# Kernel tuning notes

Measured on AMD Instinct MI355X. Metric: run time of the kernel, lower is better.

## Reference

```python
import math
import jax, jax.numpy as jnp
import numpy as np

N, L, D = 64, 128, 768          # batch, n_in capsules, feature dim
IN_DIM, OUT_DIM, N_OUT = 64, 64, 32
EPS = 1e-8

def _xavier(k, shape):
    # torch xavier_uniform: fan_in = shape[1]*prod(shape[2:]), fan_out = shape[0]*prod(shape[2:])
    rec = int(np.prod(shape[2:])) if len(shape) > 2 else 1
    fan_in, fan_out = shape[-2] * rec, shape[-1] * rec
    a = math.sqrt(6.0 / (fan_in + fan_out))
    return jax.random.uniform(k, shape, jnp.float32, -a, a)

def setup_inputs() -> dict:
    key = jax.random.key(0)
    ks = jax.random.split(key, 4)
    return {
        "x": jax.random.normal(ks[0], (N, L, D), jnp.float32),
        "Wscore": _xavier(ks[1], (L, D, 1)),
        "Bscore": jnp.zeros((L, 1, 1), jnp.float32),
        "Wcap": _xavier(ks[2], (L, D, IN_DIM)),
        "Bcap": jnp.zeros((L, 1, IN_DIM), jnp.float32),
        "Wvote": _xavier(ks[3], (L, N_OUT, IN_DIM, OUT_DIM)),
        "Bvote": jnp.zeros((L, N_OUT, 1, OUT_DIM), jnp.float32),
        "beta_use": jnp.zeros((L, 1, 1, 1), jnp.float32),
        "beta_ign": jnp.zeros((1, N_OUT, 1, 1), jnp.float32),
        "iters": 3,
    }

def reference(x, Wscore, Bscore, Wcap, Bcap, Wvote, Bvote, beta_use, beta_ign, iters):
    n_out = Wvote.shape[1]
    pi = jnp.asarray(math.pi, x.dtype)
    x_t = jnp.transpose(x, (1, 0, 2))                     # (L, N, D)
    a_in = jnp.matmul(x_t, Wscore) + Bscore               # (L, N, 1)
    mu_in = jax.nn.gelu(jnp.matmul(x_t, Wcap) + Bcap, approximate=False)  # (L, N, in_dim)
    f_a_in = jax.nn.sigmoid(a_in)[:, None, :, :]          # (L, 1, N, 1)
    # votes: (L, n_out, N, out_dim)
    V = jnp.einsum('lni,loij->lonj', mu_in, Wvote) + Bvote

    def em_step(R):
        D_use = f_a_in * R                                # (L, n_out, N, 1)
        D_ign = f_a_in - D_use
        a_out = jnp.sum(beta_use * D_use, axis=0) - jnp.sum(beta_ign * D_ign, axis=0)  # (n_out, N, 1)
        denom = jnp.sum(D_use, axis=0) + EPS              # (n_out, N, 1)
        mu_out = jnp.sum(D_use * V, axis=0) / denom       # (n_out, N, out_dim)
        var_out = jnp.sum(D_use * (V - mu_out[None]) ** 2, axis=0) / denom
        return a_out, mu_out, var_out

    R = jnp.full((1, n_out, 1, 1), 1.0 / n_out, dtype=x.dtype)
    a_out, mu_out, var_out = em_step(R)
    for _ in range(int(iters) - 1):
        # Gaussian log-likelihood of each vote under each output capsule
        log_p = (-jnp.sum((V - mu_out[None]) ** 2 / (2.0 * var_out[None] + EPS), axis=-1)
                 - 1.0 - 0.5 * pi
                 - 0.5 * jnp.sum(jnp.log(var_out[None] + EPS), axis=-1))   # (L, n_out, N)
        R = jax.nn.softmax(jax.nn.log_sigmoid(a_out)[None] + log_p[..., None], axis=1)
        a_out, mu_out, var_out = em_step(R)

    a_out = jnp.transpose(a_out[..., 0], (1, 0))          # (N, n_out)
    mu_out = jnp.transpose(mu_out, (1, 0, 2))             # (N, n_out, out_dim)
    return a_out, mu_out
```

## Files before the change

kernel.cpp:

```cpp
#include <hip/hip_runtime.h>
#include <math.h>

#define NB 64
#define LL 128
#define DD 768
#define ID 64
#define OD 64
#define NO 32
#define EPSF 1e-8f


__device__ __forceinline__ float gelu_exact(float v) {
  return 0.5f * v * (1.0f + erff(v * 0.70710678118654752440f));
}
__device__ __forceinline__ float sigmoidf_(float z) {
  return 1.0f / (1.0f + __expf(-z));
}

__global__ __launch_bounds__(256) void k0a_proj(
    const float* __restrict__ x, const float* __restrict__ Wscore,
    const float* __restrict__ Wcap,
    float* __restrict__ Cpart, float* __restrict__ apart)
{
  const int l  = blockIdx.x & 127;
  const int kc = blockIdx.x >> 7;
  const int t = threadIdx.x;
  const int tn = t >> 4;
  const int ti = t & 15;
  __shared__ float Xs[64][68];
  __shared__ float Ws[64][68];
  __shared__ float Ss[64];
  float C[4][4] = {{0.f}};
  float asum[4] = {0.f, 0.f, 0.f, 0.f};

  for (int kt = 0; kt < 2; ++kt) {
    const int kbase = kc * 128 + kt * 64;
#pragma unroll
    for (int r = 0; r < 4; ++r) {
      const int flat = r * 1024 + t * 4;
      const int p = flat >> 6, qq = flat & 63;
      *(float4*)&Xs[p][qq] = *(const float4*)&x[(p * LL + l) * DD + kbase + qq];
      *(float4*)&Ws[p][qq] = *(const float4*)&Wcap[(l * DD + kbase + p) * ID + qq];
    }
    if (t < 16)
      *(float4*)&Ss[4 * t] = *(const float4*)&Wscore[l * DD + kbase + 4 * t];
    __syncthreads();
#pragma unroll 8
    for (int k = 0; k < 64; ++k) {
      float av[4];
      av[0] = Xs[4 * tn + 0][k];
      av[1] = Xs[4 * tn + 1][k];
      av[2] = Xs[4 * tn + 2][k];
      av[3] = Xs[4 * tn + 3][k];
      const float4 b = *(const float4*)&Ws[k][4 * ti];
      const float sk = Ss[k];
#pragma unroll
      for (int a = 0; a < 4; ++a) {
        C[a][0] = fmaf(av[a], b.x, C[a][0]);
        C[a][1] = fmaf(av[a], b.y, C[a][1]);
        C[a][2] = fmaf(av[a], b.z, C[a][2]);
        C[a][3] = fmaf(av[a], b.w, C[a][3]);
        asum[a] = fmaf(av[a], sk, asum[a]);
      }
    }
    __syncthreads();
  }
#pragma unroll
  for (int a = 0; a < 4; ++a)
    *(float4*)&Cpart[kc * 524288 + (l * 64 + 4 * tn + a) * 64 + 4 * ti] =
        make_float4(C[a][0], C[a][1], C[a][2], C[a][3]);
  if (ti == 0) {
#pragma unroll
    for (int a = 0; a < 4; ++a)
      apart[kc * 8192 + l * 64 + 4 * tn + a] = asum[a];
  }
}

__global__ __launch_bounds__(256) void k0b_reduce(
    const float* __restrict__ Cpart, const float* __restrict__ Bcap,
    float* __restrict__ mu_in)
{
  const int e = (blockIdx.x * 256 + threadIdx.x) * 4;
  float4 s = *(const float4*)&Cpart[e];
#pragma unroll
  for (int kc = 1; kc < 6; ++kc) {
    const float4 p = *(const float4*)&Cpart[kc * 524288 + e];
    s.x += p.x; s.y += p.y; s.z += p.z; s.w += p.w;
  }
  const int l = e >> 12;
  const int col = e & 63;
  const float4 bc = *(const float4*)&Bcap[l * 64 + col];
  float4 g;
  g.x = gelu_exact(s.x + bc.x);
  g.y = gelu_exact(s.y + bc.y);
  g.z = gelu_exact(s.z + bc.z);
  g.w = gelu_exact(s.w + bc.w);
  *(float4*)&mu_in[e] = g;
}

__global__ __launch_bounds__(256) void k0c_fa(
    const float* __restrict__ apart, const float* __restrict__ Bscore,
    float* __restrict__ f_a)
{
  const int e = blockIdx.x * 256 + threadIdx.x;
  float s = 0.f;
#pragma unroll
  for (int kc = 0; kc < 6; ++kc) s += apart[kc * 8192 + e];
  const int l = e >> 6;
  f_a[e] = sigmoidf_(s + Bscore[l]);
}

__global__ __launch_bounds__(256) void k1_votes(
    const float* __restrict__ mu_in, const float* __restrict__ Wvote,
    const float* __restrict__ Bvote, const float* __restrict__ f_a,
    float* __restrict__ V, float* __restrict__ S1p, float* __restrict__ S2p)
{
  const int o = blockIdx.x & 31;
  const int c = blockIdx.x >> 5;
  const int t = threadIdx.x;
  const int tn = t >> 4, tj = t & 15;
  __shared__ float As[64][68];
  __shared__ float Bs[64][68];
  float s1[4][4] = {{0.f}}, s2acc[4][4] = {{0.f}};

  for (int l = c * 8; l < c * 8 + 8; ++l) {
#pragma unroll
    for (int r = 0; r < 4; ++r) {
      const int flat = r * 1024 + t * 4;
      const int p = flat >> 6, qq = flat & 63;
      *(float4*)&As[p][qq] = *(const float4*)&mu_in[(l * NB + p) * ID + qq];
      *(float4*)&Bs[p][qq] = *(const float4*)&Wvote[((l * NO + o) * ID + p) * OD + qq];
    }
    __syncthreads();
    float C[4][4] = {{0.f}};
#pragma unroll 8
    for (int k = 0; k < 64; ++k) {
      float av[4];
      av[0] = As[4 * tn + 0][k];
      av[1] = As[4 * tn + 1][k];
      av[2] = As[4 * tn + 2][k];
      av[3] = As[4 * tn + 3][k];
      const float4 b = *(const float4*)&Bs[k][4 * tj];
#pragma unroll
      for (int a = 0; a < 4; ++a) {
        C[a][0] = fmaf(av[a], b.x, C[a][0]);
        C[a][1] = fmaf(av[a], b.y, C[a][1]);
        C[a][2] = fmaf(av[a], b.z, C[a][2]);
        C[a][3] = fmaf(av[a], b.w, C[a][3]);
      }
    }
    __syncthreads();
    const float4 bv = *(const float4*)&Bvote[(l * NO + o) * OD + 4 * tj];
    float wN[4];
#pragma unroll
    for (int a = 0; a < 4; ++a)
      wN[a] = f_a[l * NB + 4 * tn + a] * (1.0f / NO);
#pragma unroll
    for (int a = 0; a < 4; ++a) {
      float4 vv;
      vv.x = C[a][0] + bv.x;
      vv.y = C[a][1] + bv.y;
      vv.z = C[a][2] + bv.z;
      vv.w = C[a][3] + bv.w;
      *(float4*)&V[((4 * tn + a) * LL + l) * (NO * OD) + o * OD + 4 * tj] = vv;
      s1[a][0] = fmaf(wN[a], vv.x, s1[a][0]);
      s1[a][1] = fmaf(wN[a], vv.y, s1[a][1]);
      s1[a][2] = fmaf(wN[a], vv.z, s1[a][2]);
      s1[a][3] = fmaf(wN[a], vv.w, s1[a][3]);
      s2acc[a][0] = fmaf(wN[a] * vv.x, vv.x, s2acc[a][0]);
      s2acc[a][1] = fmaf(wN[a] * vv.y, vv.y, s2acc[a][1]);
      s2acc[a][2] = fmaf(wN[a] * vv.z, vv.z, s2acc[a][2]);
      s2acc[a][3] = fmaf(wN[a] * vv.w, vv.w, s2acc[a][3]);
    }
  }
#pragma unroll
  for (int a = 0; a < 4; ++a) {
    const int base = ((c * NB + 4 * tn + a) * NO + o) * OD + 4 * tj;
    *(float4*)&S1p[base] = make_float4(s1[a][0], s1[a][1], s1[a][2], s1[a][3]);
    *(float4*)&S2p[base] = make_float4(s2acc[a][0], s2acc[a][1], s2acc[a][2], s2acc[a][3]);
  }
}

__global__ __launch_bounds__(256) void k2_fin1(
    const float* __restrict__ S1p, const float* __restrict__ S2p,
    const float* __restrict__ f_a, const float* __restrict__ beta_use,
    const float* __restrict__ beta_ign,
    float* __restrict__ mu_s, float* __restrict__ i2v_s, float* __restrict__ cterm)
{
  const int n = blockIdx.x;
  const int t = threadIdx.x;
  const int o = t >> 3, q = t & 7;
  const int j0 = q * 8;
  __shared__ float rA[128], rB[128];
  if (t < 128) {
    const float fv = f_a[t * NB + n];
    rA[t] = fv;
    rB[t] = beta_use[t] * fv;
  }
  __syncthreads();
  for (int s = 64; s >= 1; s >>= 1) {
    if (t < s) { rA[t] += rA[t + s]; rB[t] += rB[t + s]; }
    __syncthreads();
  }
  const float Fsum = rA[0], BUsum = rB[0];
  const float S0 = Fsum * (1.0f / NO);
  const float denom = S0 + EPSF;
  const float inv_den = 1.0f / denom;

  float S1[8], S2[8];
#pragma unroll
  for (int k = 0; k < 8; ++k) { S1[k] = 0.f; S2[k] = 0.f; }
  for (int cc = 0; cc < 16; ++cc) {
    const int base = ((cc * NB + n) * NO + o) * OD + j0;
    const float4 u0 = *(const float4*)&S1p[base];
    const float4 u1 = *(const float4*)&S1p[base + 4];
    const float4 w0 = *(const float4*)&S2p[base];
    const float4 w1 = *(const float4*)&S2p[base + 4];
    S1[0] += u0.x; S1[1] += u0.y; S1[2] += u0.z; S1[3] += u0.w;
    S1[4] += u1.x; S1[5] += u1.y; S1[6] += u1.z; S1[7] += u1.w;
    S2[0] += w0.x; S2[1] += w0.y; S2[2] += w0.z; S2[3] += w0.w;
    S2[4] += w1.x; S2[5] += w1.y; S2[6] += w1.z; S2[7] += w1.w;
  }
  float mu[8], i2v[8];
  float lacc = 0.f;
#pragma unroll
  for (int k = 0; k < 8; ++k) {
    mu[k] = S1[k] * inv_den;
    float var = (S2[k] - 2.0f * mu[k] * S1[k] + mu[k] * mu[k] * S0) * inv_den;
    var = fmaxf(var, 0.0f);
    i2v[k] = 1.0f / (2.0f * var + EPSF);
    lacc += logf(var + EPSF);
  }
  *(float4*)&mu_s[n * 2048 + t * 8]      = make_float4(mu[0], mu[1], mu[2], mu[3]);
  *(float4*)&mu_s[n * 2048 + t * 8 + 4]  = make_float4(mu[4], mu[5], mu[6], mu[7]);
  *(float4*)&i2v_s[n * 2048 + t * 8]     = make_float4(i2v[0], i2v[1], i2v[2], i2v[3]);
  *(float4*)&i2v_s[n * 2048 + t * 8 + 4] = make_float4(i2v[4], i2v[5], i2v[6], i2v[7]);
  lacc += __shfl_xor(lacc, 1);
  lacc += __shfl_xor(lacc, 2);
  lacc += __shfl_xor(lacc, 4);
  const float bI = beta_ign[o];
  const float aout = BUsum * (1.0f / NO) - bI * (Fsum - S0);
  const float lsg = fminf(aout, 0.0f) - log1pf(__expf(-fabsf(aout)));
  if (q == 0) cterm[n * NO + o] = lsg - 0.5f * lacc;
}

__global__ __launch_bounds__(256) void k3_em(
    const float* __restrict__ V, const float* __restrict__ f_a,
    const float* __restrict__ beta_use, const float* __restrict__ mu_s,
    const float* __restrict__ i2v_s, const float* __restrict__ cterm,
    float* __restrict__ S1p, float* __restrict__ S2p,
    float* __restrict__ dnp, float* __restrict__ aUp)
{
  const int n = blockIdx.x >> 3;
  const int c = blockIdx.x & 7;
  const int t = threadIdx.x;
  const int o = t >> 3, q = t & 7;
  __shared__ float ttl[2][32];

  float mu8[8], iv8[8];
  {
    const float4 a0 = *(const float4*)&mu_s[n * 2048 + t * 8];
    const float4 a1 = *(const float4*)&mu_s[n * 2048 + t * 8 + 4];
    mu8[0] = a0.x; mu8[1] = a0.y; mu8[2] = a0.z; mu8[3] = a0.w;
    mu8[4] = a1.x; mu8[5] = a1.y; mu8[6] = a1.z; mu8[7] = a1.w;
    const float4 b0 = *(const float4*)&i2v_s[n * 2048 + t * 8];
    const float4 b1 = *(const float4*)&i2v_s[n * 2048 + t * 8 + 4];
    iv8[0] = b0.x; iv8[1] = b0.y; iv8[2] = b0.z; iv8[3] = b0.w;
    iv8[4] = b1.x; iv8[5] = b1.y; iv8[6] = b1.z; iv8[7] = b1.w;
  }
  const float ct = cterm[n * NO + o];
  float aS1[8] = {0.f, 0.f, 0.f, 0.f, 0.f, 0.f, 0.f, 0.f};
  float aS2[8] = {0.f, 0.f, 0.f, 0.f, 0.f, 0.f, 0.f, 0.f};
  float dn = 0.f, aU = 0.f;

  for (int l = c * 16; l < c * 16 + 16; ++l) {
    const float4 v0 = *(const float4*)&V[(n * LL + l) * 2048 + t * 8];
    const float4 v1 = *(const float4*)&V[(n * LL + l) * 2048 + t * 8 + 4];
    float Vv[8] = {v0.x, v0.y, v0.z, v0.w, v1.x, v1.y, v1.z, v1.w};
    const float fa = f_a[l * NB + n];
    const float bu = beta_use[l];
    float d8[8];
    float s2 = 0.f;
#pragma unroll
    for (int k = 0; k < 8; ++k) {
      d8[k] = Vv[k] - mu8[k];
      s2 = fmaf(d8[k] * d8[k], iv8[k], s2);
    }
    s2 += __shfl_xor(s2, 1);
    s2 += __shfl_xor(s2, 2);
    s2 += __shfl_xor(s2, 4);
    const float tt = ct - s2;
    const int p = l & 1;
    if (q == 0) ttl[p][o] = tt;
    __syncthreads();
    const float vv = ttl[p][t & 31];
    float m = vv;
#pragma unroll
    for (int msk = 1; msk <= 16; msk <<= 1) m = fmaxf(m, __shfl_xor(m, msk));
    float z = __expf(vv - m);
#pragma unroll
    for (int msk = 1; msk <= 16; msk <<= 1) z += __shfl_xor(z, msk);
    const float w = fa * __expf(tt - m) / z;
    dn += w;
    aU = fmaf(bu, w, aU);
#pragma unroll
    for (int k = 0; k < 8; ++k) {
      aS1[k] = fmaf(w, Vv[k], aS1[k]);
      aS2[k] = fmaf(w, d8[k] * d8[k], aS2[k]);
    }
  }
  const int base = ((c * NB + n) * NO + o) * OD + q * 8;
  *(float4*)&S1p[base]     = make_float4(aS1[0], aS1[1], aS1[2], aS1[3]);
  *(float4*)&S1p[base + 4] = make_float4(aS1[4], aS1[5], aS1[6], aS1[7]);
  *(float4*)&S2p[base]     = make_float4(aS2[0], aS2[1], aS2[2], aS2[3]);
  *(float4*)&S2p[base + 4] = make_float4(aS2[4], aS2[5], aS2[6], aS2[7]);
  if (q == 0) {
    dnp[(c * NB + n) * NO + o] = dn;
    aUp[(c * NB + n) * NO + o] = aU;
  }
}

__global__ __launch_bounds__(256) void k4_fin23(
    const float* __restrict__ S1p, const float* __restrict__ S2p,
    const float* __restrict__ dnp, const float* __restrict__ aUp,
    const float* __restrict__ f_a, const float* __restrict__ beta_ign,
    float* __restrict__ mu_s, float* __restrict__ i2v_s, float* __restrict__ cterm,
    float* __restrict__ out, const int final_iter)
{
  const int n = blockIdx.x;
  const int t = threadIdx.x;
  const int o = t >> 3, q = t & 7;
  const int j0 = q * 8;
  __shared__ float rA[128];
  if (t < 128) rA[t] = f_a[t * NB + n];
  __syncthreads();
  for (int s = 64; s >= 1; s >>= 1) {
    if (t < s) rA[t] += rA[t + s];
    __syncthreads();
  }
  const float Fsum = rA[0];

  float dn = 0.f, aU = 0.f;
#pragma unroll
  for (int cc = 0; cc < 8; ++cc) {
    dn += dnp[(cc * NB + n) * NO + o];
    aU += aUp[(cc * NB + n) * NO + o];
  }
  const float S0 = dn;
  const float denom = dn + EPSF;
  const float inv_den = 1.0f / denom;

  float S1[8], S2[8];
#pragma unroll
  for (int k = 0; k < 8; ++k) { S1[k] = 0.f; S2[k] = 0.f; }
  for (int cc = 0; cc < 8; ++cc) {
    const int base = ((cc * NB + n) * NO + o) * OD + j0;
    const float4 u0 = *(const float4*)&S1p[base];
    const float4 u1 = *(const float4*)&S1p[base + 4];
    const float4 w0 = *(const float4*)&S2p[base];
    const float4 w1 = *(const float4*)&S2p[base + 4];
    S1[0] += u0.x; S1[1] += u0.y; S1[2] += u0.z; S1[3] += u0.w;
    S1[4] += u1.x; S1[5] += u1.y; S1[6] += u1.z; S1[7] += u1.w;
    S2[0] += w0.x; S2[1] += w0.y; S2[2] += w0.z; S2[3] += w0.w;
    S2[4] += w1.x; S2[5] += w1.y; S2[6] += w1.z; S2[7] += w1.w;
  }
  float mup[8];
  {
    const float4 a0 = *(const float4*)&mu_s[n * 2048 + t * 8];
    const float4 a1 = *(const float4*)&mu_s[n * 2048 + t * 8 + 4];
    mup[0] = a0.x; mup[1] = a0.y; mup[2] = a0.z; mup[3] = a0.w;
    mup[4] = a1.x; mup[5] = a1.y; mup[6] = a1.z; mup[7] = a1.w;
  }
  const float aout = aU - beta_ign[o] * (Fsum - dn);

  float mu[8], i2v[8];
  float lacc = 0.f;
#pragma unroll
  for (int k = 0; k < 8; ++k) {
    mu[k] = S1[k] * inv_den;
    const float dd = mu[k] - mup[k];
    float varn = S2[k] - 2.0f * dd * (S1[k] - mup[k] * S0) + dd * dd * S0;
    float var = fmaxf(varn * inv_den, 0.0f);
    i2v[k] = 1.0f / (2.0f * var + EPSF);
    lacc += logf(var + EPSF);
  }
  if (final_iter) {
    if (q == 0) out[n * NO + o] = aout;
    *(float4*)&out[2048 + n * 2048 + t * 8]     = make_float4(mu[0], mu[1], mu[2], mu[3]);
    *(float4*)&out[2048 + n * 2048 + t * 8 + 4] = make_float4(mu[4], mu[5], mu[6], mu[7]);
  } else {
    *(float4*)&mu_s[n * 2048 + t * 8]      = make_float4(mu[0], mu[1], mu[2], mu[3]);
    *(float4*)&mu_s[n * 2048 + t * 8 + 4]  = make_float4(mu[4], mu[5], mu[6], mu[7]);
    *(float4*)&i2v_s[n * 2048 + t * 8]     = make_float4(i2v[0], i2v[1], i2v[2], i2v[3]);
    *(float4*)&i2v_s[n * 2048 + t * 8 + 4] = make_float4(i2v[4], i2v[5], i2v[6], i2v[7]);
    lacc += __shfl_xor(lacc, 1);
    lacc += __shfl_xor(lacc, 2);
    lacc += __shfl_xor(lacc, 4);
    const float lsg = fminf(aout, 0.0f) - log1pf(__expf(-fabsf(aout)));
    if (q == 0) cterm[n * NO + o] = lsg - 0.5f * lacc;
  }
}

extern "C" void kernel_launch(void* const* d_in, const int* in_sizes, int n_in,
                              void* d_out, int out_size, void* d_ws, size_t ws_size,
                              hipStream_t stream) {
  const float* x        = (const float*)d_in[0];
  const float* Wscore   = (const float*)d_in[1];
  const float* Bscore   = (const float*)d_in[2];
  const float* Wcap     = (const float*)d_in[3];
  const float* Bcap     = (const float*)d_in[4];
  const float* Wvote    = (const float*)d_in[5];
  const float* Bvote    = (const float*)d_in[6];
  const float* beta_use = (const float*)d_in[7];
  const float* beta_ign = (const float*)d_in[8];
  float* out = (float*)d_out;

  float* ws    = (float*)d_ws;
  float* V     = ws;
  float* Cpart = V;
  float* apart = V + 3145728;
  float* mu_in = V + 16777216;
  float* f_a   = mu_in + 524288;
  float* S1p   = f_a + 8192;
  float* S2p   = S1p + 2097152;
  float* dnp   = S2p + 2097152;
  float* aUp   = dnp + 16384;
  float* mu_s  = aUp + 16384;
  float* i2v_s = mu_s + 131072;
  float* ct    = i2v_s + 131072;
  const size_t need = (size_t)(16777216 + 524288 + 8192 + 2 * 2097152 +
                               2 * 16384 + 2 * 131072 + 2048) * sizeof(float);
  if (ws_size < need) return;

  k0a_proj<<<768, 256, 0, stream>>>(x, Wscore, Wcap, Cpart, apart);
  k0b_reduce<<<512, 256, 0, stream>>>(Cpart, Bcap, mu_in);
  k0c_fa<<<32, 256, 0, stream>>>(apart, Bscore, f_a);
  k1_votes<<<512, 256, 0, stream>>>(mu_in, Wvote, Bvote, f_a, V, S1p, S2p);
  k2_fin1<<<64, 256, 0, stream>>>(S1p, S2p, f_a, beta_use, beta_ign, mu_s, i2v_s, ct);
  k3_em<<<512, 256, 0, stream>>>(V, f_a, beta_use, mu_s, i2v_s, ct, S1p, S2p, dnp, aUp);
  k4_fin23<<<64, 256, 0, stream>>>(S1p, S2p, dnp, aUp, f_a, beta_ign, mu_s, i2v_s, ct, out, 0);
  k3_em<<<512, 256, 0, stream>>>(V, f_a, beta_use, mu_s, i2v_s, ct, S1p, S2p, dnp, aUp);
  k4_fin23<<<64, 256, 0, stream>>>(S1p, S2p, dnp, aUp, f_a, beta_ign, mu_s, i2v_s, ct, out, 1);
}
```

Measured before the change: 269.3 us.

## Transpose mu_in for vectorized LDS reads and restructure EM kernel per-wave

```diff
diff --git a/kernel.cpp b/kernel.cpp
--- a/kernel.cpp
+++ b/kernel.cpp
@@ -78,24 +78,38 @@
 
 __global__ __launch_bounds__(256) void k0b_reduce(
     const float* __restrict__ Cpart, const float* __restrict__ Bcap,
-    float* __restrict__ mu_in)
-{
-  const int e = (blockIdx.x * 256 + threadIdx.x) * 4;
-  float4 s = *(const float4*)&Cpart[e];
-#pragma unroll
-  for (int kc = 1; kc < 6; ++kc) {
-    const float4 p = *(const float4*)&Cpart[kc * 524288 + e];
-    s.x += p.x; s.y += p.y; s.z += p.z; s.w += p.w;
-  }
-  const int l = e >> 12;
-  const int col = e & 63;
-  const float4 bc = *(const float4*)&Bcap[l * 64 + col];
-  float4 g;
-  g.x = gelu_exact(s.x + bc.x);
-  g.y = gelu_exact(s.y + bc.y);
-  g.z = gelu_exact(s.z + bc.z);
-  g.w = gelu_exact(s.w + bc.w);
-  *(float4*)&mu_in[e] = g;
+    float* __restrict__ mu_in_T)
+{
+  const int l = blockIdx.x;
+  const int t = threadIdx.x;
+  __shared__ float T[64][65];
+  const int n = t >> 2, i0 = (t & 3) * 16;
+#pragma unroll
+  for (int g = 0; g < 4; ++g) {
+    const int e = l * 4096 + n * 64 + i0 + 4 * g;
+    float4 s = *(const float4*)&Cpart[e];
+#pragma unroll
+    for (int kc = 1; kc < 6; ++kc) {
+      const float4 p = *(const float4*)&Cpart[kc * 524288 + e];
+      s.x += p.x; s.y += p.y; s.z += p.z; s.w += p.w;
+    }
+    const float4 bc = *(const float4*)&Bcap[l * 64 + i0 + 4 * g];
+    T[n][i0 + 4 * g + 0] = gelu_exact(s.x + bc.x);
+    T[n][i0 + 4 * g + 1] = gelu_exact(s.y + bc.y);
+    T[n][i0 + 4 * g + 2] = gelu_exact(s.z + bc.z);
+    T[n][i0 + 4 * g + 3] = gelu_exact(s.w + bc.w);
+  }
+  __syncthreads();
+  const int i = t >> 2, n0 = (t & 3) * 16;
+#pragma unroll
+  for (int g = 0; g < 4; ++g) {
+    float4 o4;
+    o4.x = T[n0 + 4 * g + 0][i];
+    o4.y = T[n0 + 4 * g + 1][i];
+    o4.z = T[n0 + 4 * g + 2][i];
+    o4.w = T[n0 + 4 * g + 3][i];
+    *(float4*)&mu_in_T[l * 4096 + i * 64 + n0 + 4 * g] = o4;
+  }
 }
 
 __global__ __launch_bounds__(256) void k0c_fa(
@@ -111,7 +125,7 @@
 }
 
 __global__ __launch_bounds__(256) void k1_votes(
-    const float* __restrict__ mu_in, const float* __restrict__ Wvote,
+    const float* __restrict__ mu_in_T, const float* __restrict__ Wvote,
     const float* __restrict__ Bvote, const float* __restrict__ f_a,
     float* __restrict__ V, float* __restrict__ S1p, float* __restrict__ S2p)
 {
@@ -128,25 +142,22 @@
     for (int r = 0; r < 4; ++r) {
       const int flat = r * 1024 + t * 4;
       const int p = flat >> 6, qq = flat & 63;
-      *(float4*)&As[p][qq] = *(const float4*)&mu_in[(l * NB + p) * ID + qq];
+      *(float4*)&As[p][qq] = *(const float4*)&mu_in_T[l * 4096 + p * 64 + qq];
       *(float4*)&Bs[p][qq] = *(const float4*)&Wvote[((l * NO + o) * ID + p) * OD + qq];
     }
     __syncthreads();
     float C[4][4] = {{0.f}};
 #pragma unroll 8
     for (int k = 0; k < 64; ++k) {
-      float av[4];
-      av[0] = As[4 * tn + 0][k];
-      av[1] = As[4 * tn + 1][k];
-      av[2] = As[4 * tn + 2][k];
-      av[3] = As[4 * tn + 3][k];
-      const float4 b = *(const float4*)&Bs[k][4 * tj];
+      const float4 a4 = *(const float4*)&As[k][4 * tn];
+      const float4 b4 = *(const float4*)&Bs[k][4 * tj];
+      const float av[4] = {a4.x, a4.y, a4.z, a4.w};
 #pragma unroll
       for (int a = 0; a < 4; ++a) {
-        C[a][0] = fmaf(av[a], b.x, C[a][0]);
-        C[a][1] = fmaf(av[a], b.y, C[a][1]);
-        C[a][2] = fmaf(av[a], b.z, C[a][2]);
-        C[a][3] = fmaf(av[a], b.w, C[a][3]);
+        C[a][0] = fmaf(av[a], b4.x, C[a][0]);
+        C[a][1] = fmaf(av[a], b4.y, C[a][1]);
+        C[a][2] = fmaf(av[a], b4.z, C[a][2]);
+        C[a][3] = fmaf(av[a], b4.w, C[a][3]);
       }
     }
     __syncthreads();
@@ -251,70 +262,102 @@
     float* __restrict__ S1p, float* __restrict__ S2p,
     float* __restrict__ dnp, float* __restrict__ aUp)
 {
-  const int n = blockIdx.x >> 3;
-  const int c = blockIdx.x & 7;
-  const int t = threadIdx.x;
-  const int o = t >> 3, q = t & 7;
-  __shared__ float ttl[2][32];
-
-  float mu8[8], iv8[8];
+  const int nb = blockIdx.x >> 4;
+  const int c  = blockIdx.x & 15;
+  const int w  = threadIdx.x >> 6;
+  const int lane = threadIdx.x & 63;
+  const int n = nb * 4 + w;
+  const int o = lane & 31;
+  const int h = lane >> 5;
+  const int jb = h * 32;
+
+  float mu[32], iv[32];
   {
-    const float4 a0 = *(const float4*)&mu_s[n * 2048 + t * 8];
-    const float4 a1 = *(const float4*)&mu_s[n * 2048 + t * 8 + 4];
-    mu8[0] = a0.x; mu8[1] = a0.y; mu8[2] = a0.z; mu8[3] = a0.w;
-    mu8[4] = a1.x; mu8[5] = a1.y; mu8[6] = a1.z; mu8[7] = a1.w;
-    const float4 b0 = *(const float4*)&i2v_s[n * 2048 + t * 8];
-    const float4 b1 = *(const float4*)&i2v_s[n * 2048 + t * 8 + 4];
-    iv8[0] = b0.x; iv8[1] = b0.y; iv8[2] = b0.z; iv8[3] = b0.w;
-    iv8[4] = b1.x; iv8[5] = b1.y; iv8[6] = b1.z; iv8[7] = b1.w;
+    const float* mb = mu_s  + n * 2048 + o * 64 + jb;
+    const float* vb = i2v_s + n * 2048 + o * 64 + jb;
+#pragma unroll
+    for (int g = 0; g < 8; ++g) {
+      const float4 m4 = *(const float4*)&mb[4 * g];
+      const float4 v4 = *(const float4*)&vb[4 * g];
+      mu[4 * g + 0] = m4.x; mu[4 * g + 1] = m4.y; mu[4 * g + 2] = m4.z; mu[4 * g + 3] = m4.w;
+      iv[4 * g + 0] = v4.x; iv[4 * g + 1] = v4.y; iv[4 * g + 2] = v4.z; iv[4 * g + 3] = v4.w;
+    }
   }
   const float ct = cterm[n * NO + o];
-  float aS1[8] = {0.f, 0.f, 0.f, 0.f, 0.f, 0.f, 0.f, 0.f};
-  float aS2[8] = {0.f, 0.f, 0.f, 0.f, 0.f, 0.f, 0.f, 0.f};
+  float S1[32], S2[32];
+#pragma unroll
+  for (int k = 0; k < 32; ++k) { S1[k] = 0.f; S2[k] = 0.f; }
   float dn = 0.f, aU = 0.f;
 
-  for (int l = c * 16; l < c * 16 + 16; ++l) {
-    const float4 v0 = *(const float4*)&V[(n * LL + l) * 2048 + t * 8];
-    const float4 v1 = *(const float4*)&V[(n * LL + l) * 2048 + t * 8 + 4];
-    float Vv[8] = {v0.x, v0.y, v0.z, v0.w, v1.x, v1.y, v1.z, v1.w};
-    const float fa = f_a[l * NB + n];
-    const float bu = beta_use[l];
-    float d8[8];
-    float s2 = 0.f;
-#pragma unroll
-    for (int k = 0; k < 8; ++k) {
-      d8[k] = Vv[k] - mu8[k];
-      s2 = fmaf(d8[k] * d8[k], iv8[k], s2);
-    }
-    s2 += __shfl_xor(s2, 1);
-    s2 += __shfl_xor(s2, 2);
-    s2 += __shfl_xor(s2, 4);
-    const float tt = ct - s2;
-    const int p = l & 1;
-    if (q == 0) ttl[p][o] = tt;
-    __syncthreads();
-    const float vv = ttl[p][t & 31];
-    float m = vv;
-#pragma unroll
-    for (int msk = 1; msk <= 16; msk <<= 1) m = fmaxf(m, __shfl_xor(m, msk));
-    float z = __expf(vv - m);
-#pragma unroll
-    for (int msk = 1; msk <= 16; msk <<= 1) z += __shfl_xor(z, msk);
-    const float w = fa * __expf(tt - m) / z;
-    dn += w;
-    aU = fmaf(bu, w, aU);
-#pragma unroll
-    for (int k = 0; k < 8; ++k) {
-      aS1[k] = fmaf(w, Vv[k], aS1[k]);
-      aS2[k] = fmaf(w, d8[k] * d8[k], aS2[k]);
-    }
-  }
-  const int base = ((c * NB + n) * NO + o) * OD + q * 8;
-  *(float4*)&S1p[base]     = make_float4(aS1[0], aS1[1], aS1[2], aS1[3]);
-  *(float4*)&S1p[base + 4] = make_float4(aS1[4], aS1[5], aS1[6], aS1[7]);
-  *(float4*)&S2p[base]     = make_float4(aS2[0], aS2[1], aS2[2], aS2[3]);
-  *(float4*)&S2p[base + 4] = make_float4(aS2[4], aS2[5], aS2[6], aS2[7]);
-  if (q == 0) {
+  const int l0 = c * 8;
+  float Va[32], Vb[32];
+#define LOADV(buf, l)                                                         \
+  {                                                                           \
+    const float* vr = V + ((size_t)n * LL + (l)) * 2048 + o * 64 + jb;        \
+    _Pragma("unroll")                                                         \
+    for (int g = 0; g < 8; ++g) {                                             \
+      const float4 q4 = *(const float4*)&vr[4 * g];                           \
+      buf[4 * g + 0] = q4.x; buf[4 * g + 1] = q4.y;                           \
+      buf[4 * g + 2] = q4.z; buf[4 * g + 3] = q4.w;                           \
+    }                                                                         \
+  }
+#define PROC(buf, l)                                                          \
+  {                                                                           \
+    const float fa = f_a[(l)*NB + n];                                         \
+    const float bu = beta_use[(l)];                                           \
+    float s2 = 0.f;                                                           \
+    _Pragma("unroll")                                                         \
+    for (int k = 0; k < 32; ++k) {                                            \
+      const float d = buf[k] - mu[k];                                         \
+      s2 = fmaf(d * iv[k], d, s2);                                            \
+    }                                                                         \
+    s2 += __shfl_xor(s2, 32);                                                 \
+    const float tt = ct - s2;                                                 \
+    float m = tt;                                                             \
+    m = fmaxf(m, __shfl_xor(m, 1));                                           \
+    m = fmaxf(m, __shfl_xor(m, 2));                                           \
+    m = fmaxf(m, __shfl_xor(m, 4));                                           \
+    m = fmaxf(m, __shfl_xor(m, 8));                                           \
+    m = fmaxf(m, __shfl_xor(m, 16));                                          \
+    const float e = __expf(tt - m);                                           \
+    float z = e;                                                              \
+    z += __shfl_xor(z, 1);                                                    \
+    z += __shfl_xor(z, 2);                                                    \
+    z += __shfl_xor(z, 4);                                                    \
+    z += __shfl_xor(z, 8);                                                    \
+    z += __shfl_xor(z, 16);                                                   \
+    const float wgt = fa * e / z;                                             \
+    dn += wgt;                                                                \
+    aU = fmaf(bu, wgt, aU);                                                   \
+    _Pragma("unroll")                                                         \
+    for (int k = 0; k < 32; ++k) {                                            \
+      S1[k] = fmaf(wgt, buf[k], S1[k]);                                       \
+      const float d = buf[k] - mu[k];                                         \
+      S2[k] = fmaf(wgt * d, d, S2[k]);                                        \
+    }                                                                         \
+  }
+
+  LOADV(Va, l0);
+#pragma unroll
+  for (int li = 0; li < 8; li += 2) {
+    if (li + 1 < 8) LOADV(Vb, l0 + li + 1);
+    PROC(Va, l0 + li);
+    if (li + 2 < 8) LOADV(Va, l0 + li + 2);
+    if (li + 1 < 8) PROC(Vb, l0 + li + 1);
+  }
+#undef LOADV
+#undef PROC
+
+  {
+    float* s1b = S1p + ((size_t)(c * NB + n) * NO + o) * OD + jb;
+    float* s2b = S2p + ((size_t)(c * NB + n) * NO + o) * OD + jb;
+#pragma unroll
+    for (int g = 0; g < 8; ++g) {
+      *(float4*)&s1b[4 * g] = make_float4(S1[4 * g], S1[4 * g + 1], S1[4 * g + 2], S1[4 * g + 3]);
+      *(float4*)&s2b[4 * g] = make_float4(S2[4 * g], S2[4 * g + 1], S2[4 * g + 2], S2[4 * g + 3]);
+    }
+  }
+  if (h == 0) {
     dnp[(c * NB + n) * NO + o] = dn;
     aUp[(c * NB + n) * NO + o] = aU;
   }
@@ -342,7 +385,7 @@
 
   float dn = 0.f, aU = 0.f;
 #pragma unroll
-  for (int cc = 0; cc < 8; ++cc) {
+  for (int cc = 0; cc < 16; ++cc) {
     dn += dnp[(cc * NB + n) * NO + o];
     aU += aUp[(cc * NB + n) * NO + o];
   }
@@ -353,7 +396,7 @@
   float S1[8], S2[8];
 #pragma unroll
   for (int k = 0; k < 8; ++k) { S1[k] = 0.f; S2[k] = 0.f; }
-  for (int cc = 0; cc < 8; ++cc) {
+  for (int cc = 0; cc < 16; ++cc) {
     const int base = ((cc * NB + n) * NO + o) * OD + j0;
     const float4 u0 = *(const float4*)&S1p[base];
     const float4 u1 = *(const float4*)&S1p[base + 4];
@@ -415,30 +458,30 @@
   const float* beta_ign = (const float*)d_in[8];
   float* out = (float*)d_out;
 
-  float* ws    = (float*)d_ws;
-  float* V     = ws;
-  float* Cpart = V;
-  float* apart = V + 3145728;
-  float* mu_in = V + 16777216;
-  float* f_a   = mu_in + 524288;
-  float* S1p   = f_a + 8192;
-  float* S2p   = S1p + 2097152;
-  float* dnp   = S2p + 2097152;
-  float* aUp   = dnp + 16384;
-  float* mu_s  = aUp + 16384;
-  float* i2v_s = mu_s + 131072;
-  float* ct    = i2v_s + 131072;
+  float* ws      = (float*)d_ws;
+  float* V       = ws;
+  float* Cpart   = ws;
+  float* apart   = ws + 3145728;
+  float* mu_in_T = ws + 16777216;
+  float* dnp     = mu_in_T;
+  float* aUp     = mu_in_T + 32768;
+  float* f_a     = mu_in_T + 524288;
+  float* S1p     = f_a + 8192;
+  float* S2p     = S1p + 2097152;
+  float* mu_s    = S2p + 2097152;
+  float* i2v_s   = mu_s + 131072;
+  float* ct      = i2v_s + 131072;
   const size_t need = (size_t)(16777216 + 524288 + 8192 + 2 * 2097152 +
-                               2 * 16384 + 2 * 131072 + 2048) * sizeof(float);
+                               2 * 131072 + 2048) * sizeof(float);
   if (ws_size < need) return;
 
   k0a_proj<<<768, 256, 0, stream>>>(x, Wscore, Wcap, Cpart, apart);
-  k0b_reduce<<<512, 256, 0, stream>>>(Cpart, Bcap, mu_in);
+  k0b_reduce<<<128, 256, 0, stream>>>(Cpart, Bcap, mu_in_T);
   k0c_fa<<<32, 256, 0, stream>>>(apart, Bscore, f_a);
-  k1_votes<<<512, 256, 0, stream>>>(mu_in, Wvote, Bvote, f_a, V, S1p, S2p);
+  k1_votes<<<512, 256, 0, stream>>>(mu_in_T, Wvote, Bvote, f_a, V, S1p, S2p);
   k2_fin1<<<64, 256, 0, stream>>>(S1p, S2p, f_a, beta_use, beta_ign, mu_s, i2v_s, ct);
-  k3_em<<<512, 256, 0, stream>>>(V, f_a, beta_use, mu_s, i2v_s, ct, S1p, S2p, dnp, aUp);
+  k3_em<<<256, 256, 0, stream>>>(V, f_a, beta_use, mu_s, i2v_s, ct, S1p, S2p, dnp, aUp);
   k4_fin23<<<64, 256, 0, stream>>>(S1p, S2p, dnp, aUp, f_a, beta_ign, mu_s, i2v_s, ct, out, 0);
-  k3_em<<<512, 256, 0, stream>>>(V, f_a, beta_use, mu_s, i2v_s, ct, S1p, S2p, dnp, aUp);
+  k3_em<<<256, 256, 0, stream>>>(V, f_a, beta_use, mu_s, i2v_s, ct, S1p, S2p, dnp, aUp);
   k4_fin23<<<64, 256, 0, stream>>>(S1p, S2p, dnp, aUp, f_a, beta_ign, mu_s, i2v_s, ct, out, 1);
 }
```

Result: slower. 305.5 us (+13.5%).

## Compute votes with split-bf16 MFMA and move first EM stats into k3_em

Applied to the files above, without the earlier changes.

```diff
diff --git a/kernel.cpp b/kernel.cpp
--- a/kernel.cpp
+++ b/kernel.cpp
@@ -9,12 +9,24 @@
 #define NO 32
 #define EPSF 1e-8f
 
+typedef unsigned short ushort_t;
+typedef __attribute__((ext_vector_type(8))) short bf16x8;
+typedef __attribute__((ext_vector_type(4))) float f32x4;
+
 
 __device__ __forceinline__ float gelu_exact(float v) {
   return 0.5f * v * (1.0f + erff(v * 0.70710678118654752440f));
 }
 __device__ __forceinline__ float sigmoidf_(float z) {
   return 1.0f / (1.0f + __expf(-z));
+}
+__device__ __forceinline__ unsigned short f2bf(float f) {
+  unsigned u = __float_as_uint(f);
+  unsigned r = (u + 0x7FFFu + ((u >> 16) & 1u)) >> 16;
+  return (unsigned short)r;
+}
+__device__ __forceinline__ float bf2f(unsigned short s) {
+  return __uint_as_float(((unsigned)s) << 16);
 }
 
 __global__ __launch_bounds__(256) void k0a_proj(
@@ -78,7 +90,7 @@
 
 __global__ __launch_bounds__(256) void k0b_reduce(
     const float* __restrict__ Cpart, const float* __restrict__ Bcap,
-    float* __restrict__ mu_in)
+    ushort_t* __restrict__ Ah, ushort_t* __restrict__ Al)
 {
   const int e = (blockIdx.x * 256 + threadIdx.x) * 4;
   float4 s = *(const float4*)&Cpart[e];
@@ -90,12 +102,15 @@
   const int l = e >> 12;
   const int col = e & 63;
   const float4 bc = *(const float4*)&Bcap[l * 64 + col];
-  float4 g;
-  g.x = gelu_exact(s.x + bc.x);
-  g.y = gelu_exact(s.y + bc.y);
-  g.z = gelu_exact(s.z + bc.z);
-  g.w = gelu_exact(s.w + bc.w);
-  *(float4*)&mu_in[e] = g;
+  float m[4] = {gelu_exact(s.x + bc.x), gelu_exact(s.y + bc.y),
+                gelu_exact(s.z + bc.z), gelu_exact(s.w + bc.w)};
+  ushort4 h, lo;
+  h.x = f2bf(m[0]); lo.x = f2bf(m[0] - bf2f(h.x));
+  h.y = f2bf(m[1]); lo.y = f2bf(m[1] - bf2f(h.y));
+  h.z = f2bf(m[2]); lo.z = f2bf(m[2] - bf2f(h.z));
+  h.w = f2bf(m[3]); lo.w = f2bf(m[3] - bf2f(h.w));
+  *(ushort4*)&Ah[e] = h;
+  *(ushort4*)&Al[e] = lo;
 }
 
 __global__ __launch_bounds__(256) void k0c_fa(
@@ -111,137 +126,96 @@
 }
 
 __global__ __launch_bounds__(256) void k1_votes(
-    const float* __restrict__ mu_in, const float* __restrict__ Wvote,
-    const float* __restrict__ Bvote, const float* __restrict__ f_a,
-    float* __restrict__ V, float* __restrict__ S1p, float* __restrict__ S2p)
-{
-  const int o = blockIdx.x & 31;
-  const int c = blockIdx.x >> 5;
+    const ushort_t* __restrict__ Ah, const ushort_t* __restrict__ Al,
+    const float* __restrict__ Wvote, const float* __restrict__ Bvote,
+    float* __restrict__ V)
+{
   const int t = threadIdx.x;
-  const int tn = t >> 4, tj = t & 15;
-  __shared__ float As[64][68];
-  __shared__ float Bs[64][68];
-  float s1[4][4] = {{0.f}}, s2acc[4][4] = {{0.f}};
-
-  for (int l = c * 8; l < c * 8 + 8; ++l) {
+  const int w = t >> 6;
+  const int lane = t & 63;
+  const int pair = blockIdx.x * 4 + w;
+  const int l = pair >> 5;
+  const int mr = lane & 15, q = lane >> 4;
+
+  __shared__ unsigned HL_all[4][4096];
+  unsigned* HL = HL_all[w];
+
+  bf16x8 afh[2][4], afl[2][4];
+#pragma unroll
+  for (int ks = 0; ks < 2; ++ks)
+#pragma unroll
+    for (int mt = 0; mt < 4; ++mt) {
+      const int off = l * 4096 + (16 * mt + mr) * 64 + ks * 32 + q * 8;
+      afh[ks][mt] = *(const bf16x8*)&Ah[off];
+      afl[ks][mt] = *(const bf16x8*)&Al[off];
+    }
+
+  const float* Wt = Wvote + (size_t)pair * 4096;
+#pragma unroll
+  for (int f = 0; f < 16; ++f) {
+    const float4 v4 = *(const float4*)&Wt[f * 256 + lane * 4];
+    const int i = f * 4 + q;
+    const int j0 = mr * 4;
+    const float e4[4] = {v4.x, v4.y, v4.z, v4.w};
+    unsigned pk[4];
+#pragma unroll
+    for (int d = 0; d < 4; ++d) {
+      const unsigned short hi = f2bf(e4[d]);
+      const unsigned short lo = f2bf(e4[d] - bf2f(hi));
+      pk[d] = (unsigned)hi | ((unsigned)lo << 16);
+    }
+    *(uint4*)&HL[i * 64 + j0] = make_uint4(pk[0], pk[1], pk[2], pk[3]);
+  }
+
+  f32x4 acc[4][4];
+#pragma unroll
+  for (int mt = 0; mt < 4; ++mt)
+#pragma unroll
+    for (int nt = 0; nt < 4; ++nt) {
+      f32x4 z = {0.f, 0.f, 0.f, 0.f};
+      acc[mt][nt] = z;
+    }
+
+#pragma unroll
+  for (int ks = 0; ks < 2; ++ks)
+#pragma unroll
+    for (int nt = 0; nt < 4; ++nt) {
+      const int j = 16 * nt + mr;
+      const int i0 = ks * 32 + q * 8;
+      unsigned wv[8];
+#pragma unroll
+      for (int d = 0; d < 8; ++d) wv[d] = HL[(i0 + d) * 64 + j];
+      union { ushort_t u[8]; bf16x8 v; } bh, bl;
+#pragma unroll
+      for (int d = 0; d < 8; ++d) {
+        bh.u[d] = (ushort_t)(wv[d] & 0xffffu);
+        bl.u[d] = (ushort_t)(wv[d] >> 16);
+      }
+#pragma unroll
+      for (int mt = 0; mt < 4; ++mt) {
+        acc[mt][nt] = __builtin_amdgcn_mfma_f32_16x16x32_bf16(
+            afh[ks][mt], bh.v, acc[mt][nt], 0, 0, 0);
+        acc[mt][nt] = __builtin_amdgcn_mfma_f32_16x16x32_bf16(
+            afh[ks][mt], bl.v, acc[mt][nt], 0, 0, 0);
+        acc[mt][nt] = __builtin_amdgcn_mfma_f32_16x16x32_bf16(
+            afl[ks][mt], bh.v, acc[mt][nt], 0, 0, 0);
+      }
+    }
+
+  float bv[4];
+#pragma unroll
+  for (int nt = 0; nt < 4; ++nt) bv[nt] = Bvote[pair * 64 + 16 * nt + mr];
+
+#pragma unroll
+  for (int mt = 0; mt < 4; ++mt)
 #pragma unroll
     for (int r = 0; r < 4; ++r) {
-      const int flat = r * 1024 + t * 4;
-      const int p = flat >> 6, qq = flat & 63;
-      *(float4*)&As[p][qq] = *(const float4*)&mu_in[(l * NB + p) * ID + qq];
-      *(float4*)&Bs[p][qq] = *(const float4*)&Wvote[((l * NO + o) * ID + p) * OD + qq];
-    }
-    __syncthreads();
-    float C[4][4] = {{0.f}};
-#pragma unroll 8
-    for (int k = 0; k < 64; ++k) {
-      float av[4];
-      av[0] = As[4 * tn + 0][k];
-      av[1] = As[4 * tn + 1][k];
-      av[2] = As[4 * tn + 2][k];
-      av[3] = As[4 * tn + 3][k];
-      const float4 b = *(const float4*)&Bs[k][4 * tj];
-#pragma unroll
-      for (int a = 0; a < 4; ++a) {
-        C[a][0] = fmaf(av[a], b.x, C[a][0]);
-        C[a][1] = fmaf(av[a], b.y, C[a][1]);
-        C[a][2] = fmaf(av[a], b.z, C[a][2]);
-        C[a][3] = fmaf(av[a], b.w, C[a][3]);
-      }
-    }
-    __syncthreads();
-    const float4 bv = *(const float4*)&Bvote[(l * NO + o) * OD + 4 * tj];
-    float wN[4];
-#pragma unroll
-    for (int a = 0; a < 4; ++a)
-      wN[a] = f_a[l * NB + 4 * tn + a] * (1.0f / NO);
-#pragma unroll
-    for (int a = 0; a < 4; ++a) {
-      float4 vv;
-      vv.x = C[a][0] + bv.x;
-      vv.y = C[a][1] + bv.y;
-      vv.z = C[a][2] + bv.z;
-      vv.w = C[a][3] + bv.w;
-      *(float4*)&V[((4 * tn + a) * LL + l) * (NO * OD) + o * OD + 4 * tj] = vv;
-      s1[a][0] = fmaf(wN[a], vv.x, s1[a][0]);
-      s1[a][1] = fmaf(wN[a], vv.y, s1[a][1]);
-      s1[a][2] = fmaf(wN[a], vv.z, s1[a][2]);
-      s1[a][3] = fmaf(wN[a], vv.w, s1[a][3]);
-      s2acc[a][0] = fmaf(wN[a] * vv.x, vv.x, s2acc[a][0]);
-      s2acc[a][1] = fmaf(wN[a] * vv.y, vv.y, s2acc[a][1]);
-      s2acc[a][2] = fmaf(wN[a] * vv.z, vv.z, s2acc[a][2]);
-      s2acc[a][3] = fmaf(wN[a] * vv.w, vv.w, s2acc[a][3]);
-    }
-  }
-#pragma unroll
-  for (int a = 0; a < 4; ++a) {
-    const int base = ((c * NB + 4 * tn + a) * NO + o) * OD + 4 * tj;
-    *(float4*)&S1p[base] = make_float4(s1[a][0], s1[a][1], s1[a][2], s1[a][3]);
-    *(float4*)&S2p[base] = make_float4(s2acc[a][0], s2acc[a][1], s2acc[a][2], s2acc[a][3]);
-  }
-}
-
-__global__ __launch_bounds__(256) void k2_fin1(
-    const float* __restrict__ S1p, const float* __restrict__ S2p,
-    const float* __restrict__ f_a, const float* __restrict__ beta_use,
-    const float* __restrict__ beta_ign,
-    float* __restrict__ mu_s, float* __restrict__ i2v_s, float* __restrict__ cterm)
-{
-  const int n = blockIdx.x;
-  const int t = threadIdx.x;
-  const int o = t >> 3, q = t & 7;
-  const int j0 = q * 8;
-  __shared__ float rA[128], rB[128];
-  if (t < 128) {
-    const float fv = f_a[t * NB + n];
-    rA[t] = fv;
-    rB[t] = beta_use[t] * fv;
-  }
-  __syncthreads();
-  for (int s = 64; s >= 1; s >>= 1) {
-    if (t < s) { rA[t] += rA[t + s]; rB[t] += rB[t + s]; }
-    __syncthreads();
-  }
-  const float Fsum = rA[0], BUsum = rB[0];
-  const float S0 = Fsum * (1.0f / NO);
-  const float denom = S0 + EPSF;
-  const float inv_den = 1.0f / denom;
-
-  float S1[8], S2[8];
-#pragma unroll
-  for (int k = 0; k < 8; ++k) { S1[k] = 0.f; S2[k] = 0.f; }
-  for (int cc = 0; cc < 16; ++cc) {
-    const int base = ((cc * NB + n) * NO + o) * OD + j0;
-    const float4 u0 = *(const float4*)&S1p[base];
-    const float4 u1 = *(const float4*)&S1p[base + 4];
-    const float4 w0 = *(const float4*)&S2p[base];
-    const float4 w1 = *(const float4*)&S2p[base + 4];
-    S1[0] += u0.x; S1[1] += u0.y; S1[2] += u0.z; S1[3] += u0.w;
-    S1[4] += u1.x; S1[5] += u1.y; S1[6] += u1.z; S1[7] += u1.w;
-    S2[0] += w0.x; S2[1] += w0.y; S2[2] += w0.z; S2[3] += w0.w;
-    S2[4] += w1.x; S2[5] += w1.y; S2[6] += w1.z; S2[7] += w1.w;
-  }
-  float mu[8], i2v[8];
-  float lacc = 0.f;
-#pragma unroll
-  for (int k = 0; k < 8; ++k) {
-    mu[k] = S1[k] * inv_den;
-    float var = (S2[k] - 2.0f * mu[k] * S1[k] + mu[k] * mu[k] * S0) * inv_den;
-    var = fmaxf(var, 0.0f);
-    i2v[k] = 1.0f / (2.0f * var + EPSF);
-    lacc += logf(var + EPSF);
-  }
-  *(float4*)&mu_s[n * 2048 + t * 8]      = make_float4(mu[0], mu[1], mu[2], mu[3]);
-  *(float4*)&mu_s[n * 2048 + t * 8 + 4]  = make_float4(mu[4], mu[5], mu[6], mu[7]);
-  *(float4*)&i2v_s[n * 2048 + t * 8]     = make_float4(i2v[0], i2v[1], i2v[2], i2v[3]);
-  *(float4*)&i2v_s[n * 2048 + t * 8 + 4] = make_float4(i2v[4], i2v[5], i2v[6], i2v[7]);
-  lacc += __shfl_xor(lacc, 1);
-  lacc += __shfl_xor(lacc, 2);
-  lacc += __shfl_xor(lacc, 4);
-  const float bI = beta_ign[o];
-  const float aout = BUsum * (1.0f / NO) - bI * (Fsum - S0);
-  const float lsg = fminf(aout, 0.0f) - log1pf(__expf(-fabsf(aout)));
-  if (q == 0) cterm[n * NO + o] = lsg - 0.5f * lacc;
+      const int n = 16 * mt + 4 * q + r;
+      const size_t base = (size_t)n * (LL * NO * OD) + (size_t)pair * 64;
+#pragma unroll
+      for (int nt = 0; nt < 4; ++nt)
+        V[base + 16 * nt + mr] = acc[mt][nt][r] + bv[nt];
+    }
 }
 
 __global__ __launch_bounds__(256) void k3_em(
@@ -249,16 +223,17 @@
     const float* __restrict__ beta_use, const float* __restrict__ mu_s,
     const float* __restrict__ i2v_s, const float* __restrict__ cterm,
     float* __restrict__ S1p, float* __restrict__ S2p,
-    float* __restrict__ dnp, float* __restrict__ aUp)
+    float* __restrict__ dnp, float* __restrict__ aUp, const int mode)
 {
   const int n = blockIdx.x >> 3;
   const int c = blockIdx.x & 7;
   const int t = threadIdx.x;
   const int o = t >> 3, q = t & 7;
-  __shared__ float ttl[2][32];
+  __shared__ float ttl[8][32];
 
   float mu8[8], iv8[8];
-  {
+  float ct = 0.f;
+  if (mode) {
     const float4 a0 = *(const float4*)&mu_s[n * 2048 + t * 8];
     const float4 a1 = *(const float4*)&mu_s[n * 2048 + t * 8 + 4];
     mu8[0] = a0.x; mu8[1] = a0.y; mu8[2] = a0.z; mu8[3] = a0.w;
@@ -267,46 +242,76 @@
     const float4 b1 = *(const float4*)&i2v_s[n * 2048 + t * 8 + 4];
     iv8[0] = b0.x; iv8[1] = b0.y; iv8[2] = b0.z; iv8[3] = b0.w;
     iv8[4] = b1.x; iv8[5] = b1.y; iv8[6] = b1.z; iv8[7] = b1.w;
-  }
-  const float ct = cterm[n * NO + o];
+    ct = cterm[n * NO + o];
+  }
   float aS1[8] = {0.f, 0.f, 0.f, 0.f, 0.f, 0.f, 0.f, 0.f};
   float aS2[8] = {0.f, 0.f, 0.f, 0.f, 0.f, 0.f, 0.f, 0.f};
   float dn = 0.f, aU = 0.f;
 
-  for (int l = c * 16; l < c * 16 + 16; ++l) {
-    const float4 v0 = *(const float4*)&V[(n * LL + l) * 2048 + t * 8];
-    const float4 v1 = *(const float4*)&V[(n * LL + l) * 2048 + t * 8 + 4];
-    float Vv[8] = {v0.x, v0.y, v0.z, v0.w, v1.x, v1.y, v1.z, v1.w};
-    const float fa = f_a[l * NB + n];
-    const float bu = beta_use[l];
-    float d8[8];
-    float s2 = 0.f;
-#pragma unroll
-    for (int k = 0; k < 8; ++k) {
-      d8[k] = Vv[k] - mu8[k];
-      s2 = fmaf(d8[k] * d8[k], iv8[k], s2);
-    }
-    s2 += __shfl_xor(s2, 1);
-    s2 += __shfl_xor(s2, 2);
-    s2 += __shfl_xor(s2, 4);
-    const float tt = ct - s2;
-    const int p = l & 1;
-    if (q == 0) ttl[p][o] = tt;
-    __syncthreads();
-    const float vv = ttl[p][t & 31];
-    float m = vv;
-#pragma unroll
-    for (int msk = 1; msk <= 16; msk <<= 1) m = fmaxf(m, __shfl_xor(m, msk));
-    float z = __expf(vv - m);
-#pragma unroll
-    for (int msk = 1; msk <= 16; msk <<= 1) z += __shfl_xor(z, msk);
-    const float w = fa * __expf(tt - m) / z;
-    dn += w;
-    aU = fmaf(bu, w, aU);
-#pragma unroll
-    for (int k = 0; k < 8; ++k) {
-      aS1[k] = fmaf(w, Vv[k], aS1[k]);
-      aS2[k] = fmaf(w, d8[k] * d8[k], aS2[k]);
+  for (int g = 0; g < 4; ++g) {
+    const int lb = c * 16 + g * 4;
+    float Vv[4][8], fa4[4], bu4[4], tt4[4];
+#pragma unroll
+    for (int u = 0; u < 4; ++u) {
+      const int l = lb + u;
+      const float4 v0 = *(const float4*)&V[((size_t)n * LL + l) * 2048 + t * 8];
+      const float4 v1 = *(const float4*)&V[((size_t)n * LL + l) * 2048 + t * 8 + 4];
+      Vv[u][0] = v0.x; Vv[u][1] = v0.y; Vv[u][2] = v0.z; Vv[u][3] = v0.w;
+      Vv[u][4] = v1.x; Vv[u][5] = v1.y; Vv[u][6] = v1.z; Vv[u][7] = v1.w;
+      fa4[u] = f_a[l * NB + n];
+      bu4[u] = beta_use[l];
+    }
+    if (mode) {
+#pragma unroll
+      for (int u = 0; u < 4; ++u) {
+        float s2 = 0.f;
+#pragma unroll
+        for (int k = 0; k < 8; ++k) {
+          const float d = Vv[u][k] - mu8[k];
+          s2 = fmaf(d * d, iv8[k], s2);
+        }
+        s2 += __shfl_xor(s2, 1);
+        s2 += __shfl_xor(s2, 2);
+        s2 += __shfl_xor(s2, 4);
+        tt4[u] = ct - s2;
+      }
+      const int sb = (g & 1) * 4;
+      if (q == 0) {
+#pragma unroll
+        for (int u = 0; u < 4; ++u) ttl[sb + u][o] = tt4[u];
+      }
+      __syncthreads();
+#pragma unroll
+      for (int u = 0; u < 4; ++u) {
+        const float vv = ttl[sb + u][t & 31];
+        float m = vv;
+#pragma unroll
+        for (int msk = 1; msk <= 16; msk <<= 1) m = fmaxf(m, __shfl_xor(m, msk));
+        float z = __expf(vv - m);
+#pragma unroll
+        for (int msk = 1; msk <= 16; msk <<= 1) z += __shfl_xor(z, msk);
+        const float wgt = fa4[u] * __expf(tt4[u] - m) / z;
+        dn += wgt;
+        aU = fmaf(bu4[u], wgt, aU);
+#pragma unroll
+        for (int k = 0; k < 8; ++k) {
+          const float d = Vv[u][k] - mu8[k];
+          aS1[k] = fmaf(wgt, Vv[u][k], aS1[k]);
+          aS2[k] = fmaf(wgt, d * d, aS2[k]);
+        }
+      }
+    } else {
+#pragma unroll
+      for (int u = 0; u < 4; ++u) {
+        const float wgt = fa4[u] * (1.0f / NO);
+        dn += wgt;
+        aU = fmaf(bu4[u], wgt, aU);
+#pragma unroll
+        for (int k = 0; k < 8; ++k) {
+          aS1[k] = fmaf(wgt, Vv[u][k], aS1[k]);
+          aS2[k] = fmaf(wgt * Vv[u][k], Vv[u][k], aS2[k]);
+        }
+      }
     }
   }
   const int base = ((c * NB + n) * NO + o) * OD + q * 8;
@@ -325,7 +330,7 @@
     const float* __restrict__ dnp, const float* __restrict__ aUp,
     const float* __restrict__ f_a, const float* __restrict__ beta_ign,
     float* __restrict__ mu_s, float* __restrict__ i2v_s, float* __restrict__ cterm,
-    float* __restrict__ out, const int final_iter)
+    float* __restrict__ out, const int final_iter, const int first)
 {
   const int n = blockIdx.x;
   const int t = threadIdx.x;
@@ -365,7 +370,10 @@
     S2[4] += w1.x; S2[5] += w1.y; S2[6] += w1.z; S2[7] += w1.w;
   }
   float mup[8];
-  {
+  if (first) {
+#pragma unroll
+    for (int k = 0; k < 8; ++k) mup[k] = 0.f;
+  } else {
     const float4 a0 = *(const float4*)&mu_s[n * 2048 + t * 8];
     const float4 a1 = *(const float4*)&mu_s[n * 2048 + t * 8 + 4];
     mup[0] = a0.x; mup[1] = a0.y; mup[2] = a0.z; mup[3] = a0.w;
@@ -415,30 +423,32 @@
   const float* beta_ign = (const float*)d_in[8];
   float* out = (float*)d_out;
 
-  float* ws    = (float*)d_ws;
-  float* V     = ws;
-  float* Cpart = V;
-  float* apart = V + 3145728;
-  float* mu_in = V + 16777216;
-  float* f_a   = mu_in + 524288;
-  float* S1p   = f_a + 8192;
-  float* S2p   = S1p + 2097152;
-  float* dnp   = S2p + 2097152;
-  float* aUp   = dnp + 16384;
-  float* mu_s  = aUp + 16384;
-  float* i2v_s = mu_s + 131072;
-  float* ct    = i2v_s + 131072;
-  const size_t need = (size_t)(16777216 + 524288 + 8192 + 2 * 2097152 +
+  float* ws     = (float*)d_ws;
+  float* V      = ws;
+  float* Cpart  = ws;
+  float* apart  = ws + 3145728;
+  ushort_t* Ah  = (ushort_t*)(ws + 16777216);
+  ushort_t* Al  = Ah + 524288;
+  float* f_a    = ws + 16777216 + 524288;
+  float* S1p    = f_a + 8192;
+  float* S2p    = S1p + 1048576;
+  float* dnp    = S2p + 1048576;
+  float* aUp    = dnp + 16384;
+  float* mu_s   = aUp + 16384;
+  float* i2v_s  = mu_s + 131072;
+  float* ct     = i2v_s + 131072;
+  const size_t need = (size_t)(16777216 + 524288 + 8192 + 2 * 1048576 +
                                2 * 16384 + 2 * 131072 + 2048) * sizeof(float);
   if (ws_size < need) return;
 
   k0a_proj<<<768, 256, 0, stream>>>(x, Wscore, Wcap, Cpart, apart);
-  k0b_reduce<<<512, 256, 0, stream>>>(Cpart, Bcap, mu_in);
+  k0b_reduce<<<512, 256, 0, stream>>>(Cpart, Bcap, Ah, Al);
   k0c_fa<<<32, 256, 0, stream>>>(apart, Bscore, f_a);
-  k1_votes<<<512, 256, 0, stream>>>(mu_in, Wvote, Bvote, f_a, V, S1p, S2p);
-  k2_fin1<<<64, 256, 0, stream>>>(S1p, S2p, f_a, beta_use, beta_ign, mu_s, i2v_s, ct);
-  k3_em<<<512, 256, 0, stream>>>(V, f_a, beta_use, mu_s, i2v_s, ct, S1p, S2p, dnp, aUp);
-  k4_fin23<<<64, 256, 0, stream>>>(S1p, S2p, dnp, aUp, f_a, beta_ign, mu_s, i2v_s, ct, out, 0);
-  k3_em<<<512, 256, 0, stream>>>(V, f_a, beta_use, mu_s, i2v_s, ct, S1p, S2p, dnp, aUp);
-  k4_fin23<<<64, 256, 0, stream>>>(S1p, S2p, dnp, aUp, f_a, beta_ign, mu_s, i2v_s, ct, out, 1);
-}
+  k1_votes<<<1024, 256, 0, stream>>>(Ah, Al, Wvote, Bvote, V);
+  k3_em<<<512, 256, 0, stream>>>(V, f_a, beta_use, mu_s, i2v_s, ct, S1p, S2p, dnp, aUp, 0);
+  k4_fin23<<<64, 256, 0, stream>>>(S1p, S2p, dnp, aUp, f_a, beta_ign, mu_s, i2v_s, ct, out, 0, 1);
+  k3_em<<<512, 256, 0, stream>>>(V, f_a, beta_use, mu_s, i2v_s, ct, S1p, S2p, dnp, aUp, 1);
+  k4_fin23<<<64, 256, 0, stream>>>(S1p, S2p, dnp, aUp, f_a, beta_ign, mu_s, i2v_s, ct, out, 0, 0);
+  k3_em<<<512, 256, 0, stream>>>(V, f_a, beta_use, mu_s, i2v_s, ct, S1p, S2p, dnp, aUp, 1);
+  k4_fin23<<<64, 256, 0, stream>>>(S1p, S2p, dnp, aUp, f_a, beta_ign, mu_s, i2v_s, ct, out, 1, 0);
+}
```

After: 247.3 us. 8.2% less time.
